# Optimization experiments

Hardware: AMD Instinct MI355X
Metric: run time of the kernel (lower is better)

Reference implementation:

```python
import jax, jax.numpy as jnp
import numpy as np

N_HEADS = 8
IN_FEATS = 512
SZ = IN_FEATS // N_HEADS          # per-head dim = 64
H = (N_HEADS * IN_FEATS) // SZ    # effective heads = n_heads^2 = 64
B, S = 2, 1024


def setup_inputs() -> dict:
    key = jax.random.key(0)
    ks = jax.random.split(key, 12)
    d_proj = N_HEADS * IN_FEATS
    sc_in = 1.0 / np.sqrt(IN_FEATS)
    sc_proj = 1.0 / np.sqrt(d_proj)
    return {
        "q": jax.random.normal(ks[0], (B, S, IN_FEATS), jnp.float32),
        "k": jax.random.normal(ks[1], (B, S, IN_FEATS), jnp.float32),
        "v": jax.random.normal(ks[2], (B, S, IN_FEATS), jnp.float32),
        "mask": jnp.zeros((B, S, S), dtype=bool),
        "Wq": jax.random.normal(ks[3], (IN_FEATS, d_proj), jnp.float32) * sc_in,
        "bq": jax.random.normal(ks[4], (d_proj,), jnp.float32) * sc_in,
        "Wk": jax.random.normal(ks[5], (IN_FEATS, d_proj), jnp.float32) * sc_in,
        "bk": jax.random.normal(ks[6], (d_proj,), jnp.float32) * sc_in,
        "Wv": jax.random.normal(ks[7], (IN_FEATS, d_proj), jnp.float32) * sc_in,
        "bv": jax.random.normal(ks[8], (d_proj,), jnp.float32) * sc_in,
        "Wf": jax.random.normal(ks[9], (d_proj, IN_FEATS), jnp.float32) * sc_proj,
        "bf": jax.random.normal(ks[10], (IN_FEATS,), jnp.float32) * sc_proj,
    }


def _split_heads(x):
    # [B,S,H*SZ] -> [B,H,S,SZ]  (matches torch.stack(torch.split(x, SZ, -1), dim=1))
    b, s, _ = x.shape
    return x.reshape(b, s, H, SZ).transpose(0, 2, 1, 3)


def reference(q, k, v, mask, Wq, bq, Wk, bk, Wv, bv, Wf, bf):
    qh = _split_heads(q @ Wq + bq)   # [B,H,S,SZ]
    kh = _split_heads(k @ Wk + bk)
    vh = _split_heads(v @ Wv + bv)
    scores = jnp.einsum("bhqd,bhkd->bhqk", qh, kh) / jnp.sqrt(jnp.float32(SZ))
    scores = jnp.where(mask[:, None, :, :], -jnp.inf, scores)
    attn = jax.nn.softmax(scores, axis=-1)  # dropout = identity (eval mode)
    out = jnp.einsum("bhqk,bhkd->bhqd", attn, vh)  # [B,H,S,SZ]
    out = out.transpose(0, 2, 1, 3).reshape(q.shape[0], q.shape[1], H * SZ)
    out = out @ Wf + bf
    return out, attn.sum(axis=1)
```

## Files before the change

kernel.cpp:

```cpp
#include <hip/hip_runtime.h>
#include <hip/hip_bf16.h>


typedef __bf16 bf16x8 __attribute__((ext_vector_type(8)));
typedef float f32x4 __attribute__((ext_vector_type(4)));

#define DEV __device__ __forceinline__

#define SC2 0.18033688011112042f

DEV f32x4 mfma16(bf16x8 a, bf16x8 b, f32x4 c) {
  return __builtin_amdgcn_mfma_f32_16x16x32_bf16(a, b, c, 0, 0, 0);
}

DEV void gload_lds16(const void* g, void* l) {
  __builtin_amdgcn_global_load_lds(
      (const __attribute__((address_space(1))) unsigned int*)g,
      (__attribute__((address_space(3))) unsigned int*)l, 16, 0, 0);
}

DEV unsigned short bf16bits(float f) {
  __hip_bfloat16 h = __float2bfloat16(f);
  return *reinterpret_cast<unsigned short*>(&h);
}

DEV void stage64(const __hip_bfloat16* src, size_t srcStride, __hip_bfloat16* dst,
                 int w, int lane) {
#pragma unroll
  for (int i = 0; i < 2; i++) {
    int r = i * 32 + w * 8 + (lane >> 3);
    int kg = (lane & 7) ^ (r & 7);
    gload_lds16(src + (size_t)r * srcStride + kg * 8, dst + (i * 32 + w * 8) * 64);
  }
}

DEV bf16x8 frag64(const __hip_bfloat16* tile, int row, int kg) {
  return *reinterpret_cast<const bf16x8*>(tile + row * 64 + ((kg ^ (row & 7)) * 8));
}

__global__ void cast3_kernel(const float* __restrict__ q, const float* __restrict__ k,
                             const float* __restrict__ v, __hip_bfloat16* __restrict__ qb,
                             __hip_bfloat16* __restrict__ kb,
                             __hip_bfloat16* __restrict__ vb) {
  int i = blockIdx.x * blockDim.x + threadIdx.x;
  int which = i >> 18, off = i & 0x3FFFF;
  const float* src = which == 0 ? q : which == 1 ? k : v;
  __hip_bfloat16* dst = which == 0 ? qb : which == 1 ? kb : vb;
  float4 f = reinterpret_cast<const float4*>(src)[off];
  union { unsigned short u[4]; uint2 v2; } pk;
  pk.u[0] = bf16bits(f.x); pk.u[1] = bf16bits(f.y);
  pk.u[2] = bf16bits(f.z); pk.u[3] = bf16bits(f.w);
  reinterpret_cast<uint2*>(dst)[off] = pk.v2;
}

__global__ void transpose4(const float* __restrict__ Wq, const float* __restrict__ Wk,
                           const float* __restrict__ Wv, const float* __restrict__ Wf,
                           __hip_bfloat16* __restrict__ Wqt, __hip_bfloat16* __restrict__ Wkt,
                           __hip_bfloat16* __restrict__ Wvt, __hip_bfloat16* __restrict__ Wft) {
  __shared__ float t[32][33];
  const int z = blockIdx.z;
  const float* W = z == 0 ? Wq : z == 1 ? Wk : z == 2 ? Wv : Wf;
  __hip_bfloat16* Wt = z == 0 ? Wqt : z == 1 ? Wkt : z == 2 ? Wvt : Wft;
  int K, N, n0, k0;
  if (z < 3) { K = 512; N = 4096; n0 = blockIdx.x * 32; k0 = blockIdx.y * 32; }
  else       { K = 4096; N = 512; n0 = blockIdx.y * 32; k0 = blockIdx.x * 32; }
  int tx = threadIdx.x, ty = threadIdx.y;
#pragma unroll
  for (int i = 0; i < 4; i++)
    t[ty + i * 8][tx] = W[(size_t)(k0 + ty + i * 8) * N + n0 + tx];
  __syncthreads();
#pragma unroll
  for (int i = 0; i < 4; i++)
    Wt[(size_t)(n0 + ty + i * 8) * K + k0 + tx] = __float2bfloat16(t[tx][ty + i * 8]);
}

struct GemmArgs {
  const __hip_bfloat16* A;
  const __hip_bfloat16* Bt;
  const float* bias;
  void* C;
  int mode;
};

template <int MI, int NI>
__global__ __launch_bounds__(256, 2) void gemm_bf16(GemmArgs g0, GemmArgs g1,
                                                    GemmArgs g2, int Ndim, int Kdim) {
  const GemmArgs& g = blockIdx.z == 0 ? g0 : blockIdx.z == 1 ? g1 : g2;
  constexpr int BM = 32 * MI, BN = 32 * NI;
  __shared__ __hip_bfloat16 As[BM * 64];
  __shared__ __hip_bfloat16 Bs[BN * 64];
  const int tid = threadIdx.x;
  const int lane = tid & 63, w = tid >> 6;
  const int wr = w >> 1, wc = w & 1;
  const int row0 = blockIdx.y * BM, col0 = blockIdx.x * BN;
  const int l15 = lane & 15, l16 = lane >> 4;

  f32x4 acc[MI][NI] = {};

  const int sr8 = w * 8 + (lane >> 3);
  const int sslot = lane & 7;

  for (int k0 = 0; k0 < Kdim; k0 += 64) {
    __syncthreads();
#pragma unroll
    for (int i = 0; i < MI; i++) {
      int r = i * 32 + sr8;
      int kg = sslot ^ (r & 7);
      gload_lds16(g.A + (size_t)(row0 + r) * Kdim + k0 + kg * 8,
                  As + (i * 32 + w * 8) * 64);
    }
#pragma unroll
    for (int i = 0; i < NI; i++) {
      int r = i * 32 + sr8;
      int kg = sslot ^ (r & 7);
      gload_lds16(g.Bt + (size_t)(col0 + r) * Kdim + k0 + kg * 8,
                  Bs + (i * 32 + w * 8) * 64);
    }
    asm volatile("s_waitcnt vmcnt(0)" ::: "memory");
    __syncthreads();
#pragma unroll
    for (int ks = 0; ks < 2; ks++) {
      const int kg = ks * 4 + l16;
      bf16x8 af[MI], bfr[NI];
#pragma unroll
      for (int mi = 0; mi < MI; mi++)
        af[mi] = frag64(As, wr * (16 * MI) + mi * 16 + l15, kg);
#pragma unroll
      for (int ni = 0; ni < NI; ni++)
        bfr[ni] = frag64(Bs, wc * (16 * NI) + ni * 16 + l15, kg);
      __builtin_amdgcn_s_setprio(1);
#pragma unroll
      for (int mi = 0; mi < MI; mi++)
#pragma unroll
        for (int ni = 0; ni < NI; ni++)
          acc[mi][ni] = mfma16(af[mi], bfr[ni], acc[mi][ni]);
      __builtin_amdgcn_s_setprio(0);
    }
  }
#pragma unroll
  for (int mi = 0; mi < MI; mi++) {
    const int rbase = row0 + wr * (16 * MI) + mi * 16 + l16 * 4;
#pragma unroll
    for (int ni = 0; ni < NI; ni++) {
      const int col = col0 + wc * (16 * NI) + ni * 16 + l15;
      const float bv = g.bias[col];
      if (g.mode == 0) {
#pragma unroll
        for (int rg = 0; rg < 4; rg++)
          ((__hip_bfloat16*)g.C)[(size_t)(rbase + rg) * Ndim + col] =
              __float2bfloat16(acc[mi][ni][rg] + bv);
      } else if (g.mode == 1) {
        const int b = rbase >> 10, s = rbase & 1023;
        union { unsigned short u[4]; uint2 v2; } pk;
#pragma unroll
        for (int rg = 0; rg < 4; rg++) pk.u[rg] = bf16bits(acc[mi][ni][rg] + bv);
        *reinterpret_cast<uint2*>((__hip_bfloat16*)g.C +
                                  ((size_t)b * 4096 + col) * 1024 + s) = pk.v2;
      } else {
#pragma unroll
        for (int rg = 0; rg < 4; rg++)
          ((float*)g.C)[(size_t)(rbase + rg) * Ndim + col] = acc[mi][ni][rg] + bv;
      }
    }
  }
}

__global__ __launch_bounds__(256, 4) void attn_flash(
    const __hip_bfloat16* __restrict__ Qp, const __hip_bfloat16* __restrict__ Kp,
    const __hip_bfloat16* __restrict__ Vt, __hip_bfloat16* __restrict__ ctx,
    float* __restrict__ lden) {
  const int lin = blockIdx.x;
  const int nw = (lin & 7) * 256 + (lin >> 3);
  const int bh = nw >> 4, q0 = (nw & 15) * 64;
  const int b = bh >> 6, h = bh & 63;
  __shared__ __hip_bfloat16 Qs[64 * 64];
  __shared__ __hip_bfloat16 Ks[64 * 64];
  __shared__ __hip_bfloat16 Vs[64 * 64];
  __shared__ __hip_bfloat16 Ps[4][16 * 72];
  const int tid = threadIdx.x, lane = tid & 63, w = tid >> 6;
  const int l15 = lane & 15, l16 = lane >> 4;

  const __hip_bfloat16* Qg = Qp + ((size_t)b * 1024 + q0) * 4096 + h * 64;
  const __hip_bfloat16* Kg = Kp + (size_t)b * 1024 * 4096 + h * 64;
  const __hip_bfloat16* Vg = Vt + ((size_t)b * 4096 + h * 64) * 1024;

  stage64(Qg, 4096, Qs, w, lane);

  f32x4 o[4] = {};
  float rs[4] = {0.f, 0.f, 0.f, 0.f};

  for (int kt = 0; kt < 16; kt++) {
    const int k0 = kt * 64;
    __syncthreads();
    stage64(Kg + (size_t)k0 * 4096, 4096, Ks, w, lane);
    stage64(Vg + k0, 1024, Vs, w, lane);
    asm volatile("s_waitcnt vmcnt(0)" ::: "memory");
    __syncthreads();

    f32x4 sc[4] = {};
    __builtin_amdgcn_s_setprio(1);
#pragma unroll
    for (int ks = 0; ks < 2; ks++) {
      const int kg = ks * 4 + l16;
      bf16x8 aq = frag64(Qs, w * 16 + l15, kg);
#pragma unroll
      for (int ni = 0; ni < 4; ni++)
        sc[ni] = mfma16(aq, frag64(Ks, ni * 16 + l15, kg), sc[ni]);
    }
    __builtin_amdgcn_s_setprio(0);

#pragma unroll
    for (int ni = 0; ni < 4; ni++) {
#pragma unroll
      for (int rg = 0; rg < 4; rg++) {
        float p = exp2f(sc[ni][rg] * SC2);
        rs[rg] += p;
        Ps[w][(l16 * 4 + rg) * 72 + ni * 16 + l15] = __float2bfloat16(p);
      }
    }
    asm volatile("s_waitcnt lgkmcnt(0)" ::: "memory");
    __builtin_amdgcn_sched_barrier(0);

    __builtin_amdgcn_s_setprio(1);
#pragma unroll
    for (int ks = 0; ks < 2; ks++) {
      const int kg = ks * 4 + l16;
      bf16x8 ap = *reinterpret_cast<const bf16x8*>(&Ps[w][l15 * 72 + kg * 8]);
#pragma unroll
      for (int df = 0; df < 4; df++)
        o[df] = mfma16(ap, frag64(Vs, df * 16 + l15, kg), o[df]);
    }
    __builtin_amdgcn_s_setprio(0);
  }

  float lfin[4];
#pragma unroll
  for (int rg = 0; rg < 4; rg++) {
    float s = rs[rg];
    s += __shfl_xor(s, 1);
    s += __shfl_xor(s, 2);
    s += __shfl_xor(s, 4);
    s += __shfl_xor(s, 8);
    lfin[rg] = s;
  }
  __hip_bfloat16* cg =
      ctx + ((size_t)b * 1024 + q0 + w * 16 + l16 * 4) * 4096 + h * 64 + l15;
#pragma unroll
  for (int rg = 0; rg < 4; rg++) {
    const float invl = 1.f / lfin[rg];
#pragma unroll
    for (int df = 0; df < 4; df++)
      cg[(size_t)rg * 4096 + df * 16] = __float2bfloat16(o[df][rg] * invl);
  }
  if (l15 == 0) {
#pragma unroll
    for (int rg = 0; rg < 4; rg++)
      lden[(size_t)bh * 1024 + q0 + w * 16 + l16 * 4 + rg] = log2f(lfin[rg]);
  }
}

__global__ __launch_bounds__(256, 4) void probsum(
    const __hip_bfloat16* __restrict__ Qp, const __hip_bfloat16* __restrict__ Kp,
    const float* __restrict__ lden, float* __restrict__ outA) {
  const int lin = blockIdx.x;
  const int nw = (lin & 7) * 64 + (lin >> 3);
  const int k0 = (nw & 15) * 64, q0 = ((nw >> 4) & 15) * 64, b = nw >> 8;
  __shared__ __hip_bfloat16 Qs[64 * 64];
  __shared__ __hip_bfloat16 Ks[64 * 64];
  __shared__ float Ls[64 * 64];
  const int tid = threadIdx.x, lane = tid & 63, w = tid >> 6;
  const int l15 = lane & 15, l16 = lane >> 4;

  for (int i = tid; i < 4096; i += 256) {
    int h = i >> 6, qq = i & 63;
    Ls[h * 64 + qq] = lden[(size_t)(b * 64 + h) * 1024 + q0 + qq];
  }

  f32x4 acc[4] = {};
  const int qrow = w * 16 + l16 * 4;

  for (int h = 0; h < 64; h++) {
    __syncthreads();
    stage64(Qp + ((size_t)b * 1024 + q0) * 4096 + h * 64, 4096, Qs, w, lane);
    stage64(Kp + ((size_t)b * 1024 + k0) * 4096 + h * 64, 4096, Ks, w, lane);
    asm volatile("s_waitcnt vmcnt(0)" ::: "memory");
    __syncthreads();
    f32x4 sc[4] = {};
    __builtin_amdgcn_s_setprio(1);
#pragma unroll
    for (int ks = 0; ks < 2; ks++) {
      const int kg = ks * 4 + l16;
      bf16x8 aq = frag64(Qs, w * 16 + l15, kg);
#pragma unroll
      for (int ni = 0; ni < 4; ni++)
        sc[ni] = mfma16(aq, frag64(Ks, ni * 16 + l15, kg), sc[ni]);
    }
    __builtin_amdgcn_s_setprio(0);
    float nl[4];
#pragma unroll
    for (int rg = 0; rg < 4; rg++) nl[rg] = Ls[h * 64 + qrow + rg];
#pragma unroll
    for (int ni = 0; ni < 4; ni++)
#pragma unroll
      for (int rg = 0; rg < 4; rg++)
        acc[ni][rg] += exp2f(fmaf(sc[ni][rg], SC2, -nl[rg]));
  }
  float* og = outA + ((size_t)b * 1024 + q0 + qrow) * 1024 + k0;
#pragma unroll
  for (int ni = 0; ni < 4; ni++)
#pragma unroll
    for (int rg = 0; rg < 4; rg++)
      og[(size_t)rg * 1024 + ni * 16 + l15] = acc[ni][rg];
}

extern "C" void kernel_launch(void* const* d_in, const int* in_sizes, int n_in,
                              void* d_out, int out_size, void* d_ws, size_t ws_size,
                              hipStream_t stream) {
  const float* q = (const float*)d_in[0];
  const float* k = (const float*)d_in[1];
  const float* v = (const float*)d_in[2];
  const float* Wq = (const float*)d_in[4];
  const float* bq = (const float*)d_in[5];
  const float* Wk = (const float*)d_in[6];
  const float* bk = (const float*)d_in[7];
  const float* Wv = (const float*)d_in[8];
  const float* bv = (const float*)d_in[9];
  const float* Wf = (const float*)d_in[10];
  const float* bfv = (const float*)d_in[11];
  float* out = (float*)d_out;
  float* attn_sum = out + (size_t)2048 * 512;

  char* ws = (char*)d_ws;
  auto alloc = [&](size_t bytes) {
    char* p = ws;
    ws += (bytes + 255) & ~(size_t)255;
    return p;
  };
  __hip_bfloat16* qb = (__hip_bfloat16*)alloc((size_t)2048 * 512 * 2);
  __hip_bfloat16* kb = (__hip_bfloat16*)alloc((size_t)2048 * 512 * 2);
  __hip_bfloat16* vb = (__hip_bfloat16*)alloc((size_t)2048 * 512 * 2);
  __hip_bfloat16* Wqt = (__hip_bfloat16*)alloc((size_t)4096 * 512 * 2);
  __hip_bfloat16* Wkt = (__hip_bfloat16*)alloc((size_t)4096 * 512 * 2);
  __hip_bfloat16* Wvt = (__hip_bfloat16*)alloc((size_t)4096 * 512 * 2);
  __hip_bfloat16* Wft = (__hip_bfloat16*)alloc((size_t)512 * 4096 * 2);
  __hip_bfloat16* Qp = (__hip_bfloat16*)alloc((size_t)2048 * 4096 * 2);
  __hip_bfloat16* Kp = (__hip_bfloat16*)alloc((size_t)2048 * 4096 * 2);
  __hip_bfloat16* Vt = (__hip_bfloat16*)alloc((size_t)2048 * 4096 * 2);
  __hip_bfloat16* ctx = (__hip_bfloat16*)alloc((size_t)2048 * 4096 * 2);
  float* lden = (float*)alloc((size_t)128 * 1024 * 4);

  cast3_kernel<<<3072, 256, 0, stream>>>(q, k, v, qb, kb, vb);
  transpose4<<<dim3(128, 16, 4), dim3(32, 8), 0, stream>>>(Wq, Wk, Wv, Wf, Wqt, Wkt,
                                                           Wvt, Wft);
  GemmArgs gq{qb, Wqt, bq, Qp, 0};
  GemmArgs gk{kb, Wkt, bk, Kp, 0};
  GemmArgs gv{vb, Wvt, bv, Vt, 1};
  gemm_bf16<4, 4><<<dim3(32, 16, 3), 256, 0, stream>>>(gq, gk, gv, 4096, 512);

  attn_flash<<<2048, 256, 0, stream>>>(Qp, Kp, Vt, ctx, lden);
  probsum<<<512, 256, 0, stream>>>(Qp, Kp, lden, attn_sum);

  GemmArgs gf{ctx, Wft, bfv, out, 2};
  gemm_bf16<2, 2><<<dim3(8, 32, 1), 256, 0, stream>>>(gf, gf, gf, 512, 4096);
}
```

Baseline: 220.5 us.

## Double-buffer GEMM and probsum loads, split-K output GEMM, MFMA row sums

The GEMM and probsum kernels now double-buffer their LDS tiles, so the next tile's global loads run while the current tile is computed. The output projection is split-K by 4 into fp32 partials that a new reduce kernel sums and adds the bias to, giving more blocks for the K=4096 GEMM. The softmax scale is folded into the Q projection epilogue. The flash-attention row sum now comes from an extra MFMA against a ones vector instead of scalar adds and shuffles, and probsum multiplies by a precomputed reciprocal. The costs are an extra kernel launch, extra partial-buffer traffic that reuses earlier workspace, more LDS per block, and row sums taken from bf16-rounded probabilities.

Measured after the change: 258.1 us. +17.1%, slower.

```diff
diff --git a/kernel.cpp b/kernel.cpp
--- a/kernel.cpp
+++ b/kernel.cpp
@@ -80,54 +80,65 @@
   const float* bias;
   void* C;
   int mode;
+  float scale;
 };
 
-template <int MI, int NI>
+template <int MI, int NI, int SPLITK>
 __global__ __launch_bounds__(256, 2) void gemm_bf16(GemmArgs g0, GemmArgs g1,
                                                     GemmArgs g2, int Ndim, int Kdim) {
-  const GemmArgs& g = blockIdx.z == 0 ? g0 : blockIdx.z == 1 ? g1 : g2;
+  const GemmArgs& g =
+      (SPLITK > 1) ? g0 : (blockIdx.z == 0 ? g0 : blockIdx.z == 1 ? g1 : g2);
   constexpr int BM = 32 * MI, BN = 32 * NI;
-  __shared__ __hip_bfloat16 As[BM * 64];
-  __shared__ __hip_bfloat16 Bs[BN * 64];
+  __shared__ __hip_bfloat16 As[2][BM * 64];
+  __shared__ __hip_bfloat16 Bs[2][BN * 64];
   const int tid = threadIdx.x;
   const int lane = tid & 63, w = tid >> 6;
   const int wr = w >> 1, wc = w & 1;
   const int row0 = blockIdx.y * BM, col0 = blockIdx.x * BN;
   const int l15 = lane & 15, l16 = lane >> 4;
 
+  const int kchunk = Kdim / SPLITK;
+  const int kbeg = (SPLITK > 1) ? blockIdx.z * kchunk : 0;
+  const int nt = kchunk / 64;
+
   f32x4 acc[MI][NI] = {};
 
   const int sr8 = w * 8 + (lane >> 3);
   const int sslot = lane & 7;
 
-  for (int k0 = 0; k0 < Kdim; k0 += 64) {
-    __syncthreads();
+  auto STAGE = [&](int buf, int k0) {
 #pragma unroll
     for (int i = 0; i < MI; i++) {
       int r = i * 32 + sr8;
       int kg = sslot ^ (r & 7);
       gload_lds16(g.A + (size_t)(row0 + r) * Kdim + k0 + kg * 8,
-                  As + (i * 32 + w * 8) * 64);
+                  &As[buf][(i * 32 + w * 8) * 64]);
     }
 #pragma unroll
     for (int i = 0; i < NI; i++) {
       int r = i * 32 + sr8;
       int kg = sslot ^ (r & 7);
       gload_lds16(g.Bt + (size_t)(col0 + r) * Kdim + k0 + kg * 8,
-                  Bs + (i * 32 + w * 8) * 64);
-    }
-    asm volatile("s_waitcnt vmcnt(0)" ::: "memory");
-    __syncthreads();
+                  &Bs[buf][(i * 32 + w * 8) * 64]);
+    }
+  };
+
+  STAGE(0, kbeg);
+  asm volatile("s_waitcnt vmcnt(0)" ::: "memory");
+  __syncthreads();
+  int cur = 0;
+  for (int t = 0; t < nt; ++t) {
+    if (t + 1 < nt) STAGE(cur ^ 1, kbeg + (t + 1) * 64);
 #pragma unroll
     for (int ks = 0; ks < 2; ks++) {
       const int kg = ks * 4 + l16;
       bf16x8 af[MI], bfr[NI];
 #pragma unroll
       for (int mi = 0; mi < MI; mi++)
-        af[mi] = frag64(As, wr * (16 * MI) + mi * 16 + l15, kg);
+        af[mi] = frag64(&As[cur][0], wr * (16 * MI) + mi * 16 + l15, kg);
 #pragma unroll
       for (int ni = 0; ni < NI; ni++)
-        bfr[ni] = frag64(Bs, wc * (16 * NI) + ni * 16 + l15, kg);
+        bfr[ni] = frag64(&Bs[cur][0], wc * (16 * NI) + ni * 16 + l15, kg);
       __builtin_amdgcn_s_setprio(1);
 #pragma unroll
       for (int mi = 0; mi < MI; mi++)
@@ -136,20 +147,25 @@
           acc[mi][ni] = mfma16(af[mi], bfr[ni], acc[mi][ni]);
       __builtin_amdgcn_s_setprio(0);
     }
-  }
+    asm volatile("s_waitcnt vmcnt(0)" ::: "memory");
+    __syncthreads();
+    cur ^= 1;
+  }
+
 #pragma unroll
   for (int mi = 0; mi < MI; mi++) {
     const int rbase = row0 + wr * (16 * MI) + mi * 16 + l16 * 4;
 #pragma unroll
     for (int ni = 0; ni < NI; ni++) {
       const int col = col0 + wc * (16 * NI) + ni * 16 + l15;
-      const float bv = g.bias[col];
       if (g.mode == 0) {
+        const float bv = g.bias[col];
 #pragma unroll
         for (int rg = 0; rg < 4; rg++)
           ((__hip_bfloat16*)g.C)[(size_t)(rbase + rg) * Ndim + col] =
-              __float2bfloat16(acc[mi][ni][rg] + bv);
+              __float2bfloat16((acc[mi][ni][rg] + bv) * g.scale);
       } else if (g.mode == 1) {
+        const float bv = g.bias[col];
         const int b = rbase >> 10, s = rbase & 1023;
         union { unsigned short u[4]; uint2 v2; } pk;
 #pragma unroll
@@ -157,12 +173,32 @@
         *reinterpret_cast<uint2*>((__hip_bfloat16*)g.C +
                                   ((size_t)b * 4096 + col) * 1024 + s) = pk.v2;
       } else {
+        float* base = (float*)g.C +
+                      (size_t)blockIdx.z * (size_t)(gridDim.y * BM) * Ndim;
 #pragma unroll
         for (int rg = 0; rg < 4; rg++)
-          ((float*)g.C)[(size_t)(rbase + rg) * Ndim + col] = acc[mi][ni][rg] + bv;
+          base[(size_t)(rbase + rg) * Ndim + col] = acc[mi][ni][rg];
       }
     }
   }
+}
+
+__global__ void reduce4_bias(const float* __restrict__ part,
+                             const float* __restrict__ bias,
+                             float* __restrict__ out) {
+  int i = blockIdx.x * blockDim.x + threadIdx.x;
+  const size_t S4 = (size_t)2048 * 512 / 4;
+  float4 a = reinterpret_cast<const float4*>(part)[i];
+  float4 b = reinterpret_cast<const float4*>(part)[i + S4];
+  float4 c = reinterpret_cast<const float4*>(part)[i + 2 * S4];
+  float4 d = reinterpret_cast<const float4*>(part)[i + 3 * S4];
+  float4 bv = reinterpret_cast<const float4*>(bias)[i & 127];
+  float4 r;
+  r.x = a.x + b.x + c.x + d.x + bv.x;
+  r.y = a.y + b.y + c.y + d.y + bv.y;
+  r.z = a.z + b.z + c.z + d.z + bv.z;
+  r.w = a.w + b.w + c.w + d.w + bv.w;
+  reinterpret_cast<float4*>(out)[i] = r;
 }
 
 __global__ __launch_bounds__(256, 4) void attn_flash(
@@ -186,8 +222,12 @@
 
   stage64(Qg, 4096, Qs, w, lane);
 
+  bf16x8 kones;
+#pragma unroll
+  for (int j = 0; j < 8; j++) kones[j] = (__bf16)1.0f;
+
   f32x4 o[4] = {};
-  float rs[4] = {0.f, 0.f, 0.f, 0.f};
+  f32x4 o4 = {};
 
   for (int kt = 0; kt < 16; kt++) {
     const int k0 = kt * 64;
@@ -213,8 +253,7 @@
     for (int ni = 0; ni < 4; ni++) {
 #pragma unroll
       for (int rg = 0; rg < 4; rg++) {
-        float p = exp2f(sc[ni][rg] * SC2);
-        rs[rg] += p;
+        float p = exp2f(sc[ni][rg]);
         Ps[w][(l16 * 4 + rg) * 72 + ni * 16 + l15] = __float2bfloat16(p);
       }
     }
@@ -229,25 +268,16 @@
 #pragma unroll
       for (int df = 0; df < 4; df++)
         o[df] = mfma16(ap, frag64(Vs, df * 16 + l15, kg), o[df]);
+      o4 = mfma16(ap, kones, o4);
     }
     __builtin_amdgcn_s_setprio(0);
   }
 
-  float lfin[4];
-#pragma unroll
-  for (int rg = 0; rg < 4; rg++) {
-    float s = rs[rg];
-    s += __shfl_xor(s, 1);
-    s += __shfl_xor(s, 2);
-    s += __shfl_xor(s, 4);
-    s += __shfl_xor(s, 8);
-    lfin[rg] = s;
-  }
   __hip_bfloat16* cg =
       ctx + ((size_t)b * 1024 + q0 + w * 16 + l16 * 4) * 4096 + h * 64 + l15;
 #pragma unroll
   for (int rg = 0; rg < 4; rg++) {
-    const float invl = 1.f / lfin[rg];
+    const float invl = 1.f / o4[rg];
 #pragma unroll
     for (int df = 0; df < 4; df++)
       cg[(size_t)rg * 4096 + df * 16] = __float2bfloat16(o[df][rg] * invl);
@@ -255,18 +285,18 @@
   if (l15 == 0) {
 #pragma unroll
     for (int rg = 0; rg < 4; rg++)
-      lden[(size_t)bh * 1024 + q0 + w * 16 + l16 * 4 + rg] = log2f(lfin[rg]);
-  }
-}
-
-__global__ __launch_bounds__(256, 4) void probsum(
+      lden[(size_t)bh * 1024 + q0 + w * 16 + l16 * 4 + rg] = log2f(o4[rg]);
+  }
+}
+
+__global__ __launch_bounds__(256, 3) void probsum(
     const __hip_bfloat16* __restrict__ Qp, const __hip_bfloat16* __restrict__ Kp,
     const float* __restrict__ lden, float* __restrict__ outA) {
   const int lin = blockIdx.x;
   const int nw = (lin & 7) * 64 + (lin >> 3);
   const int k0 = (nw & 15) * 64, q0 = ((nw >> 4) & 15) * 64, b = nw >> 8;
-  __shared__ __hip_bfloat16 Qs[64 * 64];
-  __shared__ __hip_bfloat16 Ks[64 * 64];
+  __shared__ __hip_bfloat16 Qs[2][64 * 64];
+  __shared__ __hip_bfloat16 Ks[2][64 * 64];
   __shared__ float Ls[64 * 64];
   const int tid = threadIdx.x, lane = tid & 63, w = tid >> 6;
   const int l15 = lane & 15, l16 = lane >> 4;
@@ -276,34 +306,42 @@
     Ls[h * 64 + qq] = lden[(size_t)(b * 64 + h) * 1024 + q0 + qq];
   }
 
+  auto STG = [&](int buf, int h) {
+    stage64(Qp + ((size_t)b * 1024 + q0) * 4096 + h * 64, 4096, Qs[buf], w, lane);
+    stage64(Kp + ((size_t)b * 1024 + k0) * 4096 + h * 64, 4096, Ks[buf], w, lane);
+  };
+
   f32x4 acc[4] = {};
   const int qrow = w * 16 + l16 * 4;
 
+  STG(0, 0);
+  asm volatile("s_waitcnt vmcnt(0)" ::: "memory");
+  __syncthreads();
+  int cur = 0;
   for (int h = 0; h < 64; h++) {
-    __syncthreads();
-    stage64(Qp + ((size_t)b * 1024 + q0) * 4096 + h * 64, 4096, Qs, w, lane);
-    stage64(Kp + ((size_t)b * 1024 + k0) * 4096 + h * 64, 4096, Ks, w, lane);
+    if (h + 1 < 64) STG(cur ^ 1, h + 1);
+    f32x4 sc[4] = {};
+    __builtin_amdgcn_s_setprio(1);
+#pragma unroll
+    for (int ks = 0; ks < 2; ks++) {
+      const int kg = ks * 4 + l16;
+      bf16x8 aq = frag64(Qs[cur], w * 16 + l15, kg);
+#pragma unroll
+      for (int ni = 0; ni < 4; ni++)
+        sc[ni] = mfma16(aq, frag64(Ks[cur], ni * 16 + l15, kg), sc[ni]);
+    }
+    __builtin_amdgcn_s_setprio(0);
+    float invl[4];
+#pragma unroll
+    for (int rg = 0; rg < 4; rg++) invl[rg] = exp2f(-Ls[h * 64 + qrow + rg]);
+#pragma unroll
+    for (int ni = 0; ni < 4; ni++)
+#pragma unroll
+      for (int rg = 0; rg < 4; rg++)
+        acc[ni][rg] = fmaf(exp2f(sc[ni][rg]), invl[rg], acc[ni][rg]);
     asm volatile("s_waitcnt vmcnt(0)" ::: "memory");
     __syncthreads();
-    f32x4 sc[4] = {};
-    __builtin_amdgcn_s_setprio(1);
-#pragma unroll
-    for (int ks = 0; ks < 2; ks++) {
-      const int kg = ks * 4 + l16;
-      bf16x8 aq = frag64(Qs, w * 16 + l15, kg);
-#pragma unroll
-      for (int ni = 0; ni < 4; ni++)
-        sc[ni] = mfma16(aq, frag64(Ks, ni * 16 + l15, kg), sc[ni]);
-    }
-    __builtin_amdgcn_s_setprio(0);
-    float nl[4];
-#pragma unroll
-    for (int rg = 0; rg < 4; rg++) nl[rg] = Ls[h * 64 + qrow + rg];
-#pragma unroll
-    for (int ni = 0; ni < 4; ni++)
-#pragma unroll
-      for (int rg = 0; rg < 4; rg++)
-        acc[ni][rg] += exp2f(fmaf(sc[ni][rg], SC2, -nl[rg]));
+    cur ^= 1;
   }
   float* og = outA + ((size_t)b * 1024 + q0 + qrow) * 1024 + k0;
 #pragma unroll
@@ -348,18 +386,20 @@
   __hip_bfloat16* Vt = (__hip_bfloat16*)alloc((size_t)2048 * 4096 * 2);
   __hip_bfloat16* ctx = (__hip_bfloat16*)alloc((size_t)2048 * 4096 * 2);
   float* lden = (float*)alloc((size_t)128 * 1024 * 4);
+  float* partial = (float*)qb;
 
   cast3_kernel<<<3072, 256, 0, stream>>>(q, k, v, qb, kb, vb);
   transpose4<<<dim3(128, 16, 4), dim3(32, 8), 0, stream>>>(Wq, Wk, Wv, Wf, Wqt, Wkt,
                                                            Wvt, Wft);
-  GemmArgs gq{qb, Wqt, bq, Qp, 0};
-  GemmArgs gk{kb, Wkt, bk, Kp, 0};
-  GemmArgs gv{vb, Wvt, bv, Vt, 1};
-  gemm_bf16<4, 4><<<dim3(32, 16, 3), 256, 0, stream>>>(gq, gk, gv, 4096, 512);
+  GemmArgs gq{qb, Wqt, bq, Qp, 0, SC2};
+  GemmArgs gk{kb, Wkt, bk, Kp, 0, 1.0f};
+  GemmArgs gv{vb, Wvt, bv, Vt, 1, 1.0f};
+  gemm_bf16<4, 4, 1><<<dim3(32, 16, 3), 256, 0, stream>>>(gq, gk, gv, 4096, 512);
 
   attn_flash<<<2048, 256, 0, stream>>>(Qp, Kp, Vt, ctx, lden);
   probsum<<<512, 256, 0, stream>>>(Qp, Kp, lden, attn_sum);
 
-  GemmArgs gf{ctx, Wft, bfv, out, 2};
-  gemm_bf16<2, 2><<<dim3(8, 32, 1), 256, 0, stream>>>(gf, gf, gf, 512, 4096);
-}
+  GemmArgs gf{ctx, Wft, bfv, partial, 3, 1.0f};
+  gemm_bf16<2, 2, 4><<<dim3(8, 32, 4), 256, 0, stream>>>(gf, gf, gf, 512, 4096);
+  reduce4_bias<<<1024, 256, 0, stream>>>(partial, bfv, out);
+}
```
